# Optimization experiments

Hardware: AMD Instinct MI355X
Metric: run time of the kernel (lower is better)

## Reference

```python
import jax, jax.numpy as jnp
import numpy as np

B, S, H, N, L = 256, 64, 512, 16, 2
OUT_BITS = 32            # ceil(log2(n)), n = 2**32
PTR_BITS = 6             # ceil(log2(seq_len)), seq_len = 64
OUT_DIM = 3 + PTR_BITS   # = 9
T = 2 * OUT_BITS - 1     # 63 sequential decode steps


def _ln(x, g, b):
    m = jnp.mean(x, -1, keepdims=True)
    v = jnp.mean((x - m) ** 2, -1, keepdims=True)
    return (x - m) * jax.lax.rsqrt(v + 1e-5) * g + b


def _s4_step(A, Bm, Cm, D, oW, ob, s, x):
    # diagonal-SSM S4 block step: s (B,H,N) recurrent state, x (B,H) input
    s2 = A * s + Bm * x[:, :, None]
    y = jnp.einsum('bhn,hn->bh', s2, Cm) + D * x
    y = jax.nn.gelu(y, approximate=False) @ oW + ob
    return s2, y


def _forward(input_seq, in_W, in_b, A, Bm, Cm, D, outW, outb, ln_g, ln_b, head_W, head_b):
    Bsz = input_seq.shape[0]
    dt = input_seq.dtype
    x = input_seq @ in_W + in_b            # (B,S,H)
    encoded = x                            # encoded_inputs saved before S4 stack
    # ---- encoder: L S4 blocks, residual + layernorm ----
    for j in range(L):
        def step(s, xt, j=j):
            return _s4_step(A[j], Bm[j], Cm[j], D[j], outW[j], outb[j], s, xt)
        s0 = jnp.zeros((Bsz, H, N), dt)
        _, ys = jax.lax.scan(step, s0, jnp.swapaxes(x, 0, 1))
        x = _ln(jnp.swapaxes(ys, 0, 1) + x, ln_g[j], ln_b[j])
    dec0 = jnp.broadcast_to(jnp.array([0.0, 0.0, 1.0], dt), (Bsz, 3))
    carry0 = (jnp.zeros((L, Bsz, H, N), dt), jnp.zeros((Bsz, H), dt), dec0)
    ones1 = jnp.ones((Bsz, 1), dt)

    def dstep(carry, i):
        states, ctx, dec_in = carry
        dp = dec_in @ in_W + in_b          # (B,H)
        xd = dp
        new_states = []
        for j in range(L):
            s2, y = _s4_step(A[j], Bm[j], Cm[j], D[j], outW[j], outb[j], states[j], xd)
            new_states.append(s2)
            res = jnp.where(i == 0, dp, y)   # torch code: residual=proj on step 0, else doubles x_dec
            xd = _ln(y + res, ln_g[j], ln_b[j])
        is_out = (i % 2) == 0
        # pointer retrieval (only applied on odd steps via where)
        o_ptr = jax.nn.sigmoid((xd + ctx) @ head_W + head_b)
        ptr = jnp.argmax(o_ptr[:, 3:3 + PTR_BITS], axis=1)            # (B,)
        ptr_vec = jnp.take_along_axis(encoded, ptr[:, None, None], axis=1)[:, 0]
        ctx = jnp.where(is_out, ctx, ctx + ptr_vec)
        out = jax.nn.sigmoid((xd + ctx) @ head_W + head_b)            # (B,OUT_DIM)
        next_char = jnp.where(is_out, (out[:, 0:1] > 0.5).astype(dt), jnp.zeros((Bsz, 1), dt))
        tag0 = jnp.where(is_out, 1.0, 0.0) * ones1
        tag1 = ones1 - tag0
        dec_next = jnp.concatenate([next_char, tag0, tag1], axis=1)   # (B,3)
        return (jnp.stack(new_states), ctx, dec_next), out

    _, outs = jax.lax.scan(dstep, carry0, jnp.arange(T))
    return jnp.swapaxes(outs, 0, 1)        # (B, T, OUT_DIM)


def setup_inputs() -> dict:
    ks = jax.random.split(jax.random.key(0), 8)
    f32 = jnp.float32
    return {
        'input_seq': jax.random.uniform(ks[0], (B, S, 3), f32),
        'autoregressive_steps': T,
        'in_W': jax.random.normal(ks[1], (3, H), f32) * 0.5,
        'in_b': jnp.zeros((H,), f32),
        'A': jax.random.uniform(ks[2], (L, H, N), f32, 0.5, 0.99),
        'Bm': jax.random.normal(ks[3], (L, H, N), f32) * 0.1,
        'Cm': jax.random.normal(ks[4], (L, H, N), f32) * 0.1,
        'D': jnp.ones((L, H), f32),
        'outW': jax.random.normal(ks[5], (L, H, H), f32) * 0.02,
        'outb': jnp.zeros((L, H), f32),
        'ln_g': jnp.ones((L, H), f32),
        'ln_b': jnp.zeros((L, H), f32),
        'head_W': jax.random.normal(ks[6], (H, OUT_DIM), f32) * 0.05,
        'head_b': jnp.zeros((OUT_DIM,), f32),
    }


def reference(input_seq, autoregressive_steps, in_W, in_b, A, Bm, Cm, D, outW, outb, ln_g, ln_b, head_W, head_b):
    return _forward(input_seq, in_W, in_b, A, Bm, Cm, D, outW, outb, ln_g, ln_b, head_W, head_b)
```

## Files before the change

### kernel.cpp

```cpp
#include <hip/hip_runtime.h>
#include <math.h>

#define HDIM   512
#define NDIM   16
#define SEQ    64
#define TSTEPS 63
#define BATCH  256
#define ODIM   9
#define NTHR   512


__device__ __forceinline__ float gelu_f32(float x) {
    return 0.5f * x * (1.0f + erff(x * 0.70710678118654752440f));
}

__device__ __forceinline__ float sig32(float x) {
    return 1.0f / (1.0f + expf(-x));
}

__global__ __launch_bounds__(NTHR, 2)
void s4_decode_kernel(
    const float* __restrict__ input_seq,
    const float* __restrict__ in_W,
    const float* __restrict__ in_b,
    const float* __restrict__ Aarr,
    const float* __restrict__ Barr,
    const float* __restrict__ Carr,
    const float* __restrict__ Darr,
    const float* __restrict__ outW,
    const float* __restrict__ outb,
    const float* __restrict__ ln_g,
    const float* __restrict__ ln_b,
    const float* __restrict__ headW,
    const float* __restrict__ headb,
    float* __restrict__ out,
    float* gws, float* zws,
    unsigned* fg, unsigned* fz)
{
    __shared__ float  ld_xd[HDIM];
    __shared__ float  ld_gall[4 * HDIM];
    __shared__ float4 ld_z4[16 * 4 * 32];
    __shared__ float  ld_D0[HDIM];
    __shared__ float  ld_D1[HDIM];
    __shared__ float  ld_red[16];
    __shared__ float  ld_hred[8 * ODIM];
    __shared__ float  ld_logit[ODIM + 1];
    __shared__ float  ld_dec[4];
    __shared__ int    ld_ptr;

    const int b    = blockIdx.x;
    const int tid  = threadIdx.x;
    const int hg   = tid >> 4;
    const int n    = tid & 15;
    const int mem  = (b >> 3) & 3;
    const int gbase = b - 8 * mem;
    const int c4   = tid & 31;
    const int rg   = tid >> 5;
    const int rgE  = (rg + ((b * 5) & 15)) & 15;
    const int base_row = rgE * 32;

    float s0[16], s1[16];
    float A0[16], B0[16], C0[16], A1[16], B1[16], C1[16];
    #pragma unroll
    for (int k = 0; k < 16; ++k) {
        int h  = hg + 32 * k;
        int i0 = h * NDIM + n;
        int i1 = (HDIM + h) * NDIM + n;
        A0[k] = Aarr[i0]; B0[k] = Barr[i0]; C0[k] = Carr[i0];
        A1[k] = Aarr[i1]; B1[k] = Barr[i1]; C1[k] = Carr[i1];
        s0[k] = 0.f; s1[k] = 0.f;
    }

    const float inb_t = in_b[tid];
    const float w0 = in_W[tid], w1 = in_W[HDIM + tid], w2 = in_W[2 * HDIM + tid];
    const float ob0 = outb[tid], ob1 = outb[HDIM + tid];
    const float lg0 = ln_g[tid], lg1 = ln_g[HDIM + tid];
    const float lb0 = ln_b[tid], lb1 = ln_b[HDIM + tid];

    ld_D0[tid] = Darr[tid];
    ld_D1[tid] = Darr[HDIM + tid];

    const float4* Wsl = (const float4*)outW + mem * 32 + c4;

    float ctxr = 0.f;
    if (tid == 0) { ld_dec[0] = 0.f; ld_dec[1] = 0.f; ld_dec[2] = 1.f; }
    __syncthreads();

    for (int i = 0; i < TSTEPS; ++i) {
        float dpv = fmaf(ld_dec[0], w0, fmaf(ld_dec[1], w1, fmaf(ld_dec[2], w2, inb_t)));
        __syncthreads();
        ld_xd[tid] = dpv;
        __syncthreads();

        #pragma unroll 1
        for (int blk = 0; blk < 2; ++blk) {
            const unsigned seq = (unsigned)(2 * i + blk + 1);
            {
                float* s  = blk ? s1 : s0;
                float* Ar = blk ? A1 : A0;
                float* Br = blk ? B1 : B0;
                float* Cr = blk ? C1 : C0;
                const float* Dl = blk ? ld_D1 : ld_D0;
                #pragma unroll
                for (int k = 0; k < 16; ++k) {
                    int h = hg + 32 * k;
                    float xh = ld_xd[h];
                    float sv = fmaf(Ar[k], s[k], Br[k] * xh);
                    s[k] = sv;
                    float p = sv * Cr[k];
                    p += __shfl_xor(p, 1);
                    p += __shfl_xor(p, 2);
                    p += __shfl_xor(p, 4);
                    p += __shfl_xor(p, 8);
                    if (n == 0) ld_gall[mem * HDIM + h] = gelu_f32(p + Dl[h] * xh);
                }
            }
            __syncthreads();
            __hip_atomic_store(&gws[b * HDIM + tid], ld_gall[mem * HDIM + tid],
                               __ATOMIC_RELAXED, __HIP_MEMORY_SCOPE_AGENT);
            __syncthreads();
            if (tid == 0) {
                __hip_atomic_store(&fg[b], seq, __ATOMIC_RELAXED, __HIP_MEMORY_SCOPE_AGENT);
                #pragma unroll
                for (int j = 0; j < 4; ++j) {
                    if (j == mem) continue;
                    while (__hip_atomic_load(&fg[gbase + 8 * j],
                                             __ATOMIC_RELAXED, __HIP_MEMORY_SCOPE_AGENT) < seq)
                        __builtin_amdgcn_s_sleep(1);
                }
            }
            __syncthreads();
            #pragma unroll
            for (int j = 0; j < 4; ++j) {
                if (j == mem) continue;
                ld_gall[j * HDIM + tid] =
                    __hip_atomic_load(&gws[(gbase + 8 * j) * HDIM + tid],
                                      __ATOMIC_RELAXED, __HIP_MEMORY_SCOPE_AGENT);
            }
            __syncthreads();
            {
                const float4* Wb = Wsl + (size_t)blk * HDIM * 128;
                float4 acc[4];
                #pragma unroll
                for (int bi = 0; bi < 4; ++bi) acc[bi] = make_float4(0.f, 0.f, 0.f, 0.f);
                float4 a0 = Wb[(size_t)(base_row)     * 128];
                float4 a1 = Wb[(size_t)(base_row + 1) * 128];
                #pragma unroll 2
                for (int rr = 0; rr < 32; rr += 4) {
                    int rB = base_row + ((rr + 2) & 31);
                    float4 b0 = Wb[(size_t)rB * 128];
                    float4 b1 = Wb[(size_t)(rB + 1) * 128];
                    {
                        int r = base_row + rr;
                        #pragma unroll
                        for (int bi = 0; bi < 4; ++bi) {
                            float g0 = ld_gall[bi * HDIM + r];
                            float g1 = ld_gall[bi * HDIM + r + 1];
                            acc[bi].x = fmaf(g1, a1.x, fmaf(g0, a0.x, acc[bi].x));
                            acc[bi].y = fmaf(g1, a1.y, fmaf(g0, a0.y, acc[bi].y));
                            acc[bi].z = fmaf(g1, a1.z, fmaf(g0, a0.z, acc[bi].z));
                            acc[bi].w = fmaf(g1, a1.w, fmaf(g0, a0.w, acc[bi].w));
                        }
                    }
                    int rA = base_row + ((rr + 4) & 31);
                    a0 = Wb[(size_t)rA * 128];
                    a1 = Wb[(size_t)(rA + 1) * 128];
                    {
                        int r = base_row + rr + 2;
                        #pragma unroll
                        for (int bi = 0; bi < 4; ++bi) {
                            float g0 = ld_gall[bi * HDIM + r];
                            float g1 = ld_gall[bi * HDIM + r + 1];
                            acc[bi].x = fmaf(g1, b1.x, fmaf(g0, b0.x, acc[bi].x));
                            acc[bi].y = fmaf(g1, b1.y, fmaf(g0, b0.y, acc[bi].y));
                            acc[bi].z = fmaf(g1, b1.z, fmaf(g0, b0.z, acc[bi].z));
                            acc[bi].w = fmaf(g1, b1.w, fmaf(g0, b0.w, acc[bi].w));
                        }
                    }
                }
                #pragma unroll
                for (int bi = 0; bi < 4; ++bi)
                    ld_z4[(rg * 4 + bi) * 32 + c4] = acc[bi];
            }
            __syncthreads();
            {
                const float* zf = (const float*)ld_z4;
                int bi2 = tid >> 7;
                int col = tid & 127;
                float zv = 0.f;
                #pragma unroll
                for (int k = 0; k < 16; ++k) zv += zf[(k * 4 + bi2) * 128 + col];
                __hip_atomic_store(&zws[(gbase + 8 * bi2) * HDIM + mem * 128 + col], zv,
                                   __ATOMIC_RELAXED, __HIP_MEMORY_SCOPE_AGENT);
            }
            __syncthreads();
            if (tid == 0) {
                __hip_atomic_store(&fz[b], seq, __ATOMIC_RELAXED, __HIP_MEMORY_SCOPE_AGENT);
                #pragma unroll
                for (int j = 0; j < 4; ++j) {
                    if (j == mem) continue;
                    while (__hip_atomic_load(&fz[gbase + 8 * j],
                                             __ATOMIC_RELAXED, __HIP_MEMORY_SCOPE_AGENT) < seq)
                        __builtin_amdgcn_s_sleep(1);
                }
            }
            __syncthreads();
            {
                float z = __hip_atomic_load(&zws[b * HDIM + tid],
                                            __ATOMIC_RELAXED, __HIP_MEMORY_SCOPE_AGENT)
                        + (blk ? ob1 : ob0);
                float res = (i == 0) ? dpv : z;
                float tmp = z + res;
                float v1 = tmp, v2 = tmp * tmp;
                #pragma unroll
                for (int m = 1; m < 64; m <<= 1) {
                    v1 += __shfl_xor(v1, m);
                    v2 += __shfl_xor(v2, m);
                }
                if ((tid & 63) == 0) {
                    ld_red[2 * (tid >> 6)]     = v1;
                    ld_red[2 * (tid >> 6) + 1] = v2;
                }
                __syncthreads();
                float s1r = 0.f, s2r = 0.f;
                #pragma unroll
                for (int q = 0; q < 8; ++q) { s1r += ld_red[2*q]; s2r += ld_red[2*q+1]; }
                float mu  = s1r * (1.f / 512.f);
                float var = s2r * (1.f / 512.f) - mu * mu;
                float rs  = rsqrtf(var + 1e-5f);
                __syncthreads();
                ld_xd[tid] = (tmp - mu) * rs * (blk ? lg1 : lg0) + (blk ? lb1 : lb0);
                __syncthreads();
            }
        }

        {
            float v = ld_xd[tid] + ctxr;
            const float* w = headW + tid * ODIM;
            float p[ODIM];
            #pragma unroll
            for (int o = 0; o < ODIM; ++o) p[o] = v * w[o];
            #pragma unroll
            for (int m = 1; m < 64; m <<= 1) {
                #pragma unroll
                for (int o = 0; o < ODIM; ++o) p[o] += __shfl_xor(p[o], m);
            }
            if ((tid & 63) == 0) {
                int wv = tid >> 6;
                #pragma unroll
                for (int o = 0; o < ODIM; ++o) ld_hred[wv * ODIM + o] = p[o];
            }
            __syncthreads();
            if (tid < ODIM) {
                float s = headb[tid];
                #pragma unroll
                for (int wv = 0; wv < 8; ++wv) s += ld_hred[wv * ODIM + tid];
                ld_logit[tid] = s;
            }
            __syncthreads();
        }

        const bool is_out = ((i & 1) == 0);
        if (is_out) {
            if (tid < ODIM)
                out[(b * TSTEPS + i) * ODIM + tid] = sig32(ld_logit[tid]);
            if (tid == 0) {
                float nc = (sig32(ld_logit[0]) > 0.5f) ? 1.f : 0.f;
                ld_dec[0] = nc; ld_dec[1] = 1.f; ld_dec[2] = 0.f;
            }
            __syncthreads();
        } else {
            if (tid == 0) {
                int best = 0; float bv = sig32(ld_logit[3]);
                #pragma unroll
                for (int o = 1; o < 6; ++o) {
                    float v2 = sig32(ld_logit[3 + o]);
                    if (v2 > bv) { bv = v2; best = o; }
                }
                ld_ptr = best;
                ld_dec[0] = 0.f; ld_dec[1] = 0.f; ld_dec[2] = 1.f;
            }
            __syncthreads();
            {
                const float* iseq = input_seq + (b * SEQ + ld_ptr) * 3;
                float e0 = iseq[0], e1 = iseq[1], e2 = iseq[2];
                ctxr += fmaf(e0, w0, fmaf(e1, w1, fmaf(e2, w2, inb_t)));
            }
            __syncthreads();
            {
                float v = ld_xd[tid] + ctxr;
                const float* w = headW + tid * ODIM;
                float p[ODIM];
                #pragma unroll
                for (int o = 0; o < ODIM; ++o) p[o] = v * w[o];
                #pragma unroll
                for (int m = 1; m < 64; m <<= 1) {
                    #pragma unroll
                    for (int o = 0; o < ODIM; ++o) p[o] += __shfl_xor(p[o], m);
                }
                if ((tid & 63) == 0) {
                    int wv = tid >> 6;
                    #pragma unroll
                    for (int o = 0; o < ODIM; ++o) ld_hred[wv * ODIM + o] = p[o];
                }
                __syncthreads();
                if (tid < ODIM) {
                    float s = headb[tid];
                    #pragma unroll
                    for (int wv = 0; wv < 8; ++wv) s += ld_hred[wv * ODIM + tid];
                    out[(b * TSTEPS + i) * ODIM + tid] = sig32(s);
                }
            }
            __syncthreads();
        }
    }
}

extern "C" void kernel_launch(void* const* d_in, const int* in_sizes, int n_in,
                              void* d_out, int out_size, void* d_ws, size_t ws_size,
                              hipStream_t stream) {
    (void)in_sizes; (void)n_in; (void)ws_size; (void)out_size;
    const float* input_seq = (const float*)d_in[0];
    const float* in_W   = (const float*)d_in[2];
    const float* in_b   = (const float*)d_in[3];
    const float* Aarr   = (const float*)d_in[4];
    const float* Barr   = (const float*)d_in[5];
    const float* Carr   = (const float*)d_in[6];
    const float* Darr   = (const float*)d_in[7];
    const float* outW   = (const float*)d_in[8];
    const float* outb   = (const float*)d_in[9];
    const float* ln_g   = (const float*)d_in[10];
    const float* ln_b   = (const float*)d_in[11];
    const float* headW  = (const float*)d_in[12];
    const float* headb  = (const float*)d_in[13];
    float* out = (float*)d_out;

    unsigned* fg = (unsigned*)d_ws;
    unsigned* fz = fg + BATCH;
    float* gws = (float*)((char*)d_ws + 4096);
    float* zws = gws + BATCH * HDIM;

    hipMemsetAsync(d_ws, 0, 4096, stream);

    s4_decode_kernel<<<BATCH, NTHR, 0, stream>>>(
        input_seq, in_W, in_b, Aarr, Barr, Carr, Darr,
        outW, outb, ln_g, ln_b, headW, headb, out,
        gws, zws, fg, fz);
}
```

Measured before the change: 1.550 ms.

## Detect same-XCD block groups and use L2-scoped loads/stores for exchange

At kernel start, each block publishes its XCC id and checks whether its three partner blocks run on the same XCD. If they do, the gws/zws exchange uses plain stores and sc0 (L2-coherent) inline-asm loads instead of agent-scope atomics. Flag polling is also spread over three threads, one per partner, instead of one thread looping over all three. This targets cross-block handoff latency, but adds an initial handshake and relies on L2 coherence within an XCD, which depends on how blocks are scheduled.

Result: faster. 1.363 ms (-12.1%).

```diff
diff --git a/kernel.cpp b/kernel.cpp
--- a/kernel.cpp
+++ b/kernel.cpp
@@ -16,6 +16,26 @@
 
 __device__ __forceinline__ float sig32(float x) {
     return 1.0f / (1.0f + expf(-x));
+}
+
+__device__ __forceinline__ void load3_l2(const float* p0, const float* p1,
+                                         const float* p2,
+                                         float& v0, float& v1, float& v2) {
+    asm volatile(
+        "global_load_dword %0, %3, off sc0\n\t"
+        "global_load_dword %1, %4, off sc0\n\t"
+        "global_load_dword %2, %5, off sc0\n\t"
+        "s_waitcnt vmcnt(0)"
+        : "=&v"(v0), "=&v"(v1), "=&v"(v2)
+        : "v"(p0), "v"(p1), "v"(p2)
+        : "memory");
+}
+__device__ __forceinline__ float load1_l2(const float* p) {
+    float v;
+    asm volatile("global_load_dword %0, %1, off sc0\n\t"
+                 "s_waitcnt vmcnt(0)"
+                 : "=v"(v) : "v"(p) : "memory");
+    return v;
 }
 
 __global__ __launch_bounds__(NTHR, 2)
@@ -35,7 +55,8 @@
     const float* __restrict__ headb,
     float* __restrict__ out,
     float* gws, float* zws,
-    unsigned* fg, unsigned* fz)
+    unsigned* fg, unsigned* fz,
+    unsigned* fx, unsigned* xid)
 {
     __shared__ float  ld_xd[HDIM];
     __shared__ float  ld_gall[4 * HDIM];
@@ -47,6 +68,7 @@
     __shared__ float  ld_logit[ODIM + 1];
     __shared__ float  ld_dec[4];
     __shared__ int    ld_ptr;
+    __shared__ int    ld_fast;
 
     const int b    = blockIdx.x;
     const int tid  = threadIdx.x;
@@ -58,6 +80,25 @@
     const int rg   = tid >> 5;
     const int rgE  = (rg + ((b * 5) & 15)) & 15;
     const int base_row = rgE * 32;
+    const int j0 = 0 + (0 >= mem), j1 = 1 + (1 >= mem), j2 = 2 + (2 >= mem);
+
+    unsigned myxcd;
+    asm volatile("s_getreg_b32 %0, hwreg(HW_REG_XCC_ID)" : "=s"(myxcd));
+    if (tid == 0) {
+        __hip_atomic_store(&xid[b], myxcd, __ATOMIC_RELAXED, __HIP_MEMORY_SCOPE_AGENT);
+        __hip_atomic_store(&fx[b], 1u, __ATOMIC_RELEASE, __HIP_MEMORY_SCOPE_AGENT);
+        unsigned ok = 1;
+        #pragma unroll
+        for (int j = 0; j < 4; ++j) {
+            if (j == mem) continue;
+            while (__hip_atomic_load(&fx[gbase + 8 * j],
+                                     __ATOMIC_ACQUIRE, __HIP_MEMORY_SCOPE_AGENT) == 0)
+                __builtin_amdgcn_s_sleep(1);
+            ok &= (__hip_atomic_load(&xid[gbase + 8 * j],
+                                     __ATOMIC_RELAXED, __HIP_MEMORY_SCOPE_AGENT) == myxcd);
+        }
+        ld_fast = (int)ok;
+    }
 
     float s0[16], s1[16];
     float A0[16], B0[16], C0[16], A1[16], B1[16], C1[16];
@@ -85,6 +126,7 @@
     float ctxr = 0.f;
     if (tid == 0) { ld_dec[0] = 0.f; ld_dec[1] = 0.f; ld_dec[2] = 1.f; }
     __syncthreads();
+    const bool fast = (ld_fast != 0);
 
     for (int i = 0; i < TSTEPS; ++i) {
         float dpv = fmaf(ld_dec[0], w0, fmaf(ld_dec[1], w1, fmaf(ld_dec[2], w2, inb_t)));
@@ -116,25 +158,39 @@
                 }
             }
             __syncthreads();
-            __hip_atomic_store(&gws[b * HDIM + tid], ld_gall[mem * HDIM + tid],
-                               __ATOMIC_RELAXED, __HIP_MEMORY_SCOPE_AGENT);
-            __syncthreads();
-            if (tid == 0) {
+            if (fast) {
+                gws[b * HDIM + tid] = ld_gall[mem * HDIM + tid];
+            } else {
+                __hip_atomic_store(&gws[b * HDIM + tid], ld_gall[mem * HDIM + tid],
+                                   __ATOMIC_RELAXED, __HIP_MEMORY_SCOPE_AGENT);
+            }
+            __syncthreads();
+            if (tid == 4)
                 __hip_atomic_store(&fg[b], seq, __ATOMIC_RELAXED, __HIP_MEMORY_SCOPE_AGENT);
-                #pragma unroll
-                for (int j = 0; j < 4; ++j) {
-                    if (j == mem) continue;
-                    while (__hip_atomic_load(&fg[gbase + 8 * j],
-                                             __ATOMIC_RELAXED, __HIP_MEMORY_SCOPE_AGENT) < seq)
-                        __builtin_amdgcn_s_sleep(1);
-                }
-            }
-            __syncthreads();
-            #pragma unroll
-            for (int j = 0; j < 4; ++j) {
-                if (j == mem) continue;
-                ld_gall[j * HDIM + tid] =
-                    __hip_atomic_load(&gws[(gbase + 8 * j) * HDIM + tid],
+            if (tid < 3) {
+                int j = tid + (tid >= mem ? 1 : 0);
+                while (__hip_atomic_load(&fg[gbase + 8 * j],
+                                         __ATOMIC_RELAXED, __HIP_MEMORY_SCOPE_AGENT) < seq)
+                    __builtin_amdgcn_s_sleep(1);
+            }
+            __syncthreads();
+            if (fast) {
+                float v0, v1, v2;
+                load3_l2(&gws[(gbase + 8 * j0) * HDIM + tid],
+                         &gws[(gbase + 8 * j1) * HDIM + tid],
+                         &gws[(gbase + 8 * j2) * HDIM + tid], v0, v1, v2);
+                ld_gall[j0 * HDIM + tid] = v0;
+                ld_gall[j1 * HDIM + tid] = v1;
+                ld_gall[j2 * HDIM + tid] = v2;
+            } else {
+                ld_gall[j0 * HDIM + tid] =
+                    __hip_atomic_load(&gws[(gbase + 8 * j0) * HDIM + tid],
+                                      __ATOMIC_RELAXED, __HIP_MEMORY_SCOPE_AGENT);
+                ld_gall[j1 * HDIM + tid] =
+                    __hip_atomic_load(&gws[(gbase + 8 * j1) * HDIM + tid],
+                                      __ATOMIC_RELAXED, __HIP_MEMORY_SCOPE_AGENT);
+                ld_gall[j2 * HDIM + tid] =
+                    __hip_atomic_load(&gws[(gbase + 8 * j2) * HDIM + tid],
                                       __ATOMIC_RELAXED, __HIP_MEMORY_SCOPE_AGENT);
             }
             __syncthreads();
@@ -190,25 +246,26 @@
                 float zv = 0.f;
                 #pragma unroll
                 for (int k = 0; k < 16; ++k) zv += zf[(k * 4 + bi2) * 128 + col];
-                __hip_atomic_store(&zws[(gbase + 8 * bi2) * HDIM + mem * 128 + col], zv,
-                                   __ATOMIC_RELAXED, __HIP_MEMORY_SCOPE_AGENT);
-            }
-            __syncthreads();
-            if (tid == 0) {
+                float* zp = &zws[(gbase + 8 * bi2) * HDIM + mem * 128 + col];
+                if (fast) *zp = zv;
+                else __hip_atomic_store(zp, zv, __ATOMIC_RELAXED, __HIP_MEMORY_SCOPE_AGENT);
+            }
+            __syncthreads();
+            if (tid == 4)
                 __hip_atomic_store(&fz[b], seq, __ATOMIC_RELAXED, __HIP_MEMORY_SCOPE_AGENT);
-                #pragma unroll
-                for (int j = 0; j < 4; ++j) {
-                    if (j == mem) continue;
-                    while (__hip_atomic_load(&fz[gbase + 8 * j],
-                                             __ATOMIC_RELAXED, __HIP_MEMORY_SCOPE_AGENT) < seq)
-                        __builtin_amdgcn_s_sleep(1);
-                }
-            }
-            __syncthreads();
-            {
-                float z = __hip_atomic_load(&zws[b * HDIM + tid],
-                                            __ATOMIC_RELAXED, __HIP_MEMORY_SCOPE_AGENT)
-                        + (blk ? ob1 : ob0);
+            if (tid < 3) {
+                int j = tid + (tid >= mem ? 1 : 0);
+                while (__hip_atomic_load(&fz[gbase + 8 * j],
+                                         __ATOMIC_RELAXED, __HIP_MEMORY_SCOPE_AGENT) < seq)
+                    __builtin_amdgcn_s_sleep(1);
+            }
+            __syncthreads();
+            {
+                float zraw = fast ? load1_l2(&zws[b * HDIM + tid])
+                                  : __hip_atomic_load(&zws[b * HDIM + tid],
+                                                      __ATOMIC_RELAXED,
+                                                      __HIP_MEMORY_SCOPE_AGENT);
+                float z = zraw + (blk ? ob1 : ob0);
                 float res = (i == 0) ? dpv : z;
                 float tmp = z + res;
                 float v1 = tmp, v2 = tmp * tmp;
@@ -335,8 +392,10 @@
     const float* headb  = (const float*)d_in[13];
     float* out = (float*)d_out;
 
-    unsigned* fg = (unsigned*)d_ws;
-    unsigned* fz = fg + BATCH;
+    unsigned* fg  = (unsigned*)d_ws;
+    unsigned* fz  = fg + BATCH;
+    unsigned* fx  = fz + BATCH;
+    unsigned* xid = fx + BATCH;
     float* gws = (float*)((char*)d_ws + 4096);
     float* zws = gws + BATCH * HDIM;
 
@@ -345,5 +404,5 @@
     s4_decode_kernel<<<BATCH, NTHR, 0, stream>>>(
         input_seq, in_W, in_b, Aarr, Barr, Carr, Darr,
         outW, outb, ln_g, ln_b, headW, headb, out,
-        gws, zws, fg, fz);
-}
+        gws, zws, fg, fz, fx, xid);
+}
```
